# Kernel tuning notes

Hardware: AMD Instinct MI355X
Metric: run time of the kernel (lower is better)

Reference implementation:

```python
import jax, jax.numpy as jnp
import numpy as np

N_NODES = 50000


def _gcn_norm(edge_index, num_nodes):
    # PyG GCNConv default: add self-loops, symmetric normalization D^-1/2 A D^-1/2
    src, dst = edge_index[0], edge_index[1]
    loops = jnp.arange(num_nodes, dtype=src.dtype)
    src = jnp.concatenate([src, loops])
    dst = jnp.concatenate([dst, loops])
    deg = jax.ops.segment_sum(jnp.ones_like(src, dtype=jnp.float32), dst,
                              num_segments=num_nodes)
    dis = jnp.where(deg > 0, jax.lax.rsqrt(jnp.maximum(deg, 1.0)), 0.0)
    norm = dis[src] * dis[dst]  # [E']
    return src, dst, norm


def _gcn_conv(x, W, b, src, dst, norm, num_nodes):
    h = x @ W                                   # [N, out] transform first
    msg = h[src] * norm[:, None]                # [E', out] gather + scale
    agg = jax.ops.segment_sum(msg, dst, num_segments=num_nodes)  # scatter-add
    return agg + b


def setup_inputs() -> dict:
    key = jax.random.key(0)
    k1, k2, k3, k4 = jax.random.split(key, 4)
    n, e, d_in, d_h = N_NODES, 800000, 256, 128
    basic_block = jax.random.normal(k1, (n, d_in), dtype=jnp.float32)
    edge_index = jax.random.randint(k2, (2, e), 0, n, dtype=jnp.int64)
    W1 = jax.random.normal(k3, (d_in, d_h), dtype=jnp.float32) * (1.0 / np.sqrt(d_in))
    b1 = jnp.zeros((d_h,), dtype=jnp.float32)
    W2 = jax.random.normal(k4, (d_h, d_h), dtype=jnp.float32) * (1.0 / np.sqrt(d_h))
    b2 = jnp.zeros((d_h,), dtype=jnp.float32)
    return {"basic_block": basic_block, "edge_index": edge_index,
            "W1": W1, "b1": b1, "W2": W2, "b2": b2}


def reference(basic_block, edge_index, W1, b1, W2, b2):
    n = basic_block.shape[0]
    src, dst, norm = _gcn_norm(edge_index, n)
    x = jax.nn.relu(_gcn_conv(basic_block, W1, b1, src, dst, norm, n))
    x = _gcn_conv(x, W2, b2, src, dst, norm, n)
    return x
```

## Files before the change

### kernel.cpp

```cpp
#include <hip/hip_runtime.h>
#include <hip/hip_bf16.h>
#include <stdint.h>

#define D_H 128
#define CAP 64

typedef __bf16 bf16_t;
typedef unsigned short u16;
typedef bf16_t bf16x8 __attribute__((ext_vector_type(8)));
typedef bf16_t bf16x4 __attribute__((ext_vector_type(4)));
typedef float  f32x4  __attribute__((ext_vector_type(4)));

__global__ void k_pref(const int* __restrict__ src, const int* __restrict__ dst,
                       int* __restrict__ cnt, u16* __restrict__ csr,
                       int E, int gcr,
                       const float* __restrict__ W1, bf16_t* __restrict__ W1h,
                       bf16_t* __restrict__ W1l, int K1,
                       const float* __restrict__ W2, bf16_t* __restrict__ W2h,
                       bf16_t* __restrict__ W2l, int K2) {
    int bx = (int)blockIdx.x;
    if (bx < gcr) {
        int e = bx * 256 + threadIdx.x;
        if (e < E) {
            int d   = dst[e];
            int pos = atomicAdd(&cnt[d], 1);
            if (pos < CAP) csr[(size_t)d * CAP + pos] = (u16)src[e];
        }
        return;
    }
    int id = (bx - gcr) * 256 + threadIdx.x;
    int n1 = K1 * 128;
    if (id < n1) {
        int k = id >> 7, n = id & 127;
        float w = W1[id];
        bf16_t h = (bf16_t)w;
        W1h[(size_t)n * K1 + k] = h;
        W1l[(size_t)n * K1 + k] = (bf16_t)(w - (float)h);
    } else if (id < n1 + K2 * 128) {
        int id2 = id - n1;
        int k = id2 >> 7, n = id2 & 127;
        float w = W2[id2];
        bf16_t h = (bf16_t)w;
        W2h[(size_t)n * K2 + k] = h;
        W2l[(size_t)n * K2 + k] = (bf16_t)(w - (float)h);
    }
}

#define LDK 40

__global__ __launch_bounds__(256) void k_mm1(
        const float* __restrict__ Af,
        const bf16_t* __restrict__ Wh, const bf16_t* __restrict__ Wl,
        const int* __restrict__ cnt, bf16_t* __restrict__ Cb,
        int N, int K) {
    __shared__ bf16_t AsH[64][LDK];
    __shared__ bf16_t AsL[64][LDK];
    __shared__ bf16_t BsH[64][LDK];
    __shared__ bf16_t BsL[64][LDK];

    const int t    = threadIdx.x;
    const int lane = t & 63;
    const int wave = t >> 6;
    const int row0 = ((int)blockIdx.x >> 1) * 64;
    const int col0 = ((int)blockIdx.x & 1) * 64;
    const int wm   = (wave & 1) * 32;
    const int wn   = (wave >> 1) * 32;
    const int fm   = lane & 15;
    const int fq   = lane >> 4;

    f32x4 acc[2][2] = {};

    for (int k0 = 0; k0 < K; k0 += 32) {
        __syncthreads();
#pragma unroll
        for (int i = 0; i < 2; i++) {
            int idx = t + i * 256;
            int r   = idx >> 3;
            int c4  = idx & 7;
            int gr  = row0 + r;
            float4 v = make_float4(0.f, 0.f, 0.f, 0.f);
            if (gr < N) v = *(const float4*)(Af + (size_t)gr * K + k0 + c4 * 4);
            bf16_t h0 = (bf16_t)v.x, h1 = (bf16_t)v.y, h2 = (bf16_t)v.z, h3 = (bf16_t)v.w;
            bf16_t l0 = (bf16_t)(v.x - (float)h0);
            bf16_t l1 = (bf16_t)(v.y - (float)h1);
            bf16_t l2 = (bf16_t)(v.z - (float)h2);
            bf16_t l3 = (bf16_t)(v.w - (float)h3);
            *(bf16x4*)&AsH[r][c4 * 4] = (bf16x4){h0, h1, h2, h3};
            *(bf16x4*)&AsL[r][c4 * 4] = (bf16x4){l0, l1, l2, l3};
        }
        {
            int r  = t >> 2;
            int c8 = t & 3;
            *(bf16x8*)&BsH[r][c8 * 8] = *(const bf16x8*)(Wh + (size_t)(col0 + r) * K + k0 + c8 * 8);
            *(bf16x8*)&BsL[r][c8 * 8] = *(const bf16x8*)(Wl + (size_t)(col0 + r) * K + k0 + c8 * 8);
        }
        __syncthreads();

        bf16x8 ah[2], al[2], bh[2], bl[2];
#pragma unroll
        for (int i = 0; i < 2; i++) {
            ah[i] = *(const bf16x8*)&AsH[wm + i * 16 + fm][fq * 8];
            al[i] = *(const bf16x8*)&AsL[wm + i * 16 + fm][fq * 8];
            bh[i] = *(const bf16x8*)&BsH[wn + i * 16 + fm][fq * 8];
            bl[i] = *(const bf16x8*)&BsL[wn + i * 16 + fm][fq * 8];
        }
#pragma unroll
        for (int mi = 0; mi < 2; mi++)
#pragma unroll
            for (int ni = 0; ni < 2; ni++) {
                acc[mi][ni] = __builtin_amdgcn_mfma_f32_16x16x32_bf16(ah[mi], bh[ni], acc[mi][ni], 0, 0, 0);
                acc[mi][ni] = __builtin_amdgcn_mfma_f32_16x16x32_bf16(ah[mi], bl[ni], acc[mi][ni], 0, 0, 0);
                acc[mi][ni] = __builtin_amdgcn_mfma_f32_16x16x32_bf16(al[mi], bh[ni], acc[mi][ni], 0, 0, 0);
            }
    }

#pragma unroll
    for (int mi = 0; mi < 2; mi++)
#pragma unroll
        for (int r = 0; r < 4; r++) {
            int grow = row0 + wm + mi * 16 + fq * 4 + r;
            if (grow < N) {
                float dr = 1.0f / sqrtf((float)(cnt[grow] + 1));
#pragma unroll
                for (int ni = 0; ni < 2; ni++)
                    Cb[(size_t)grow * D_H + col0 + wn + ni * 16 + fm] = (bf16_t)(dr * acc[mi][ni][r]);
            }
        }
}

__global__ __launch_bounds__(256) void k_mm2(const bf16_t* __restrict__ Ah,
                                             const bf16_t* __restrict__ Al,
                                             const bf16_t* __restrict__ Wh,
                                             const bf16_t* __restrict__ Wl,
                                             const int* __restrict__ cnt,
                                             bf16_t* __restrict__ Cb,
                                             int N, int K) {
    __shared__ bf16_t AsH[64][LDK];
    __shared__ bf16_t AsL[64][LDK];
    __shared__ bf16_t BsH[64][LDK];
    __shared__ bf16_t BsL[64][LDK];

    const int t    = threadIdx.x;
    const int lane = t & 63;
    const int wave = t >> 6;
    const int row0 = ((int)blockIdx.x >> 1) * 64;
    const int col0 = ((int)blockIdx.x & 1) * 64;
    const int wm   = (wave & 1) * 32;
    const int wn   = (wave >> 1) * 32;
    const int fm   = lane & 15;
    const int fq   = lane >> 4;

    f32x4 acc[2][2] = {};

    for (int k0 = 0; k0 < K; k0 += 32) {
        __syncthreads();
        {
            int r  = t >> 2;
            int c8 = t & 3;
            int gr = row0 + r;
            bf16x8 vh = {}, vl = {};
            if (gr < N) {
                vh = *(const bf16x8*)(Ah + (size_t)gr * K + k0 + c8 * 8);
                vl = *(const bf16x8*)(Al + (size_t)gr * K + k0 + c8 * 8);
            }
            *(bf16x8*)&AsH[r][c8 * 8] = vh;
            *(bf16x8*)&AsL[r][c8 * 8] = vl;
            *(bf16x8*)&BsH[r][c8 * 8] = *(const bf16x8*)(Wh + (size_t)(col0 + r) * K + k0 + c8 * 8);
            *(bf16x8*)&BsL[r][c8 * 8] = *(const bf16x8*)(Wl + (size_t)(col0 + r) * K + k0 + c8 * 8);
        }
        __syncthreads();

        bf16x8 ah[2], al[2], bh[2], bl[2];
#pragma unroll
        for (int i = 0; i < 2; i++) {
            ah[i] = *(const bf16x8*)&AsH[wm + i * 16 + fm][fq * 8];
            al[i] = *(const bf16x8*)&AsL[wm + i * 16 + fm][fq * 8];
            bh[i] = *(const bf16x8*)&BsH[wn + i * 16 + fm][fq * 8];
            bl[i] = *(const bf16x8*)&BsL[wn + i * 16 + fm][fq * 8];
        }
#pragma unroll
        for (int mi = 0; mi < 2; mi++)
#pragma unroll
            for (int ni = 0; ni < 2; ni++) {
                acc[mi][ni] = __builtin_amdgcn_mfma_f32_16x16x32_bf16(ah[mi], bh[ni], acc[mi][ni], 0, 0, 0);
                acc[mi][ni] = __builtin_amdgcn_mfma_f32_16x16x32_bf16(ah[mi], bl[ni], acc[mi][ni], 0, 0, 0);
                acc[mi][ni] = __builtin_amdgcn_mfma_f32_16x16x32_bf16(al[mi], bh[ni], acc[mi][ni], 0, 0, 0);
            }
    }

#pragma unroll
    for (int mi = 0; mi < 2; mi++)
#pragma unroll
        for (int r = 0; r < 4; r++) {
            int grow = row0 + wm + mi * 16 + fq * 4 + r;
            if (grow < N) {
                float dr = 1.0f / sqrtf((float)(cnt[grow] + 1));
#pragma unroll
                for (int ni = 0; ni < 2; ni++)
                    Cb[(size_t)grow * D_H + col0 + wn + ni * 16 + fm] = (bf16_t)(dr * acc[mi][ni][r]);
            }
        }
}

__global__ __launch_bounds__(256) void k_agg(const bf16_t* __restrict__ Hb,
                                             const int* __restrict__ cnt,
                                             const u16* __restrict__ csr,
                                             const float4* __restrict__ bias4,
                                             float4* __restrict__ outF,
                                             bf16_t* __restrict__ outH,
                                             bf16_t* __restrict__ outL,
                                             int N, int mode) {
    const int slot = threadIdx.x >> 4;
    const int lane = threadIdx.x & 15;
    const int node = blockIdx.x * 16 + slot;
    if (node >= N) return;

    const bf16_t* Hrow = Hb + (size_t)lane * 8;
    const int  deg = min(cnt[node], CAP);
    const u16* lst = csr + (size_t)node * CAP;

    float a0[8], a1[8], a2[8], a3[8];
    {
        bf16x8 v = *(const bf16x8*)(Hrow + (size_t)node * D_H);
#pragma unroll
        for (int j = 0; j < 8; j++) { a0[j] = (float)v[j]; a1[j] = 0.f; a2[j] = 0.f; a3[j] = 0.f; }
    }

    int k = 0;
    for (; k + 4 <= deg; k += 4) {
        ushort4 s4 = *(const ushort4*)(lst + k);
        bf16x8 h0 = *(const bf16x8*)(Hrow + (size_t)s4.x * D_H);
        bf16x8 h1 = *(const bf16x8*)(Hrow + (size_t)s4.y * D_H);
        bf16x8 h2 = *(const bf16x8*)(Hrow + (size_t)s4.z * D_H);
        bf16x8 h3 = *(const bf16x8*)(Hrow + (size_t)s4.w * D_H);
#pragma unroll
        for (int j = 0; j < 8; j++) {
            a0[j] += (float)h0[j];
            a1[j] += (float)h1[j];
            a2[j] += (float)h2[j];
            a3[j] += (float)h3[j];
        }
    }
    if (k + 2 <= deg) {
        int s0 = (int)lst[k], s1 = (int)lst[k + 1];
        bf16x8 h0 = *(const bf16x8*)(Hrow + (size_t)s0 * D_H);
        bf16x8 h1 = *(const bf16x8*)(Hrow + (size_t)s1 * D_H);
#pragma unroll
        for (int j = 0; j < 8; j++) { a0[j] += (float)h0[j]; a1[j] += (float)h1[j]; }
        k += 2;
    }
    if (k < deg) {
        int s0 = (int)lst[k];
        bf16x8 h0 = *(const bf16x8*)(Hrow + (size_t)s0 * D_H);
#pragma unroll
        for (int j = 0; j < 8; j++) a2[j] += (float)h0[j];
    }

    float sum[8];
#pragma unroll
    for (int j = 0; j < 8; j++) sum[j] = (a0[j] + a1[j]) + (a2[j] + a3[j]);

    const float  di = 1.0f / sqrtf((float)(deg + 1));
    const float4 b0 = bias4[lane * 2];
    const float4 b1 = bias4[lane * 2 + 1];
    float v0 = fmaf(di, sum[0], b0.x), v1 = fmaf(di, sum[1], b0.y);
    float v2 = fmaf(di, sum[2], b0.z), v3 = fmaf(di, sum[3], b0.w);
    float v4 = fmaf(di, sum[4], b1.x), v5 = fmaf(di, sum[5], b1.y);
    float v6 = fmaf(di, sum[6], b1.z), v7 = fmaf(di, sum[7], b1.w);

    if (mode == 1) {
        v0 = fmaxf(v0, 0.f); v1 = fmaxf(v1, 0.f); v2 = fmaxf(v2, 0.f); v3 = fmaxf(v3, 0.f);
        v4 = fmaxf(v4, 0.f); v5 = fmaxf(v5, 0.f); v6 = fmaxf(v6, 0.f); v7 = fmaxf(v7, 0.f);
        bf16_t h0 = (bf16_t)v0, h1 = (bf16_t)v1, h2 = (bf16_t)v2, h3 = (bf16_t)v3;
        bf16_t h4 = (bf16_t)v4, h5 = (bf16_t)v5, h6 = (bf16_t)v6, h7 = (bf16_t)v7;
        *(bf16x8*)(outH + (size_t)node * D_H + lane * 8) =
            (bf16x8){h0, h1, h2, h3, h4, h5, h6, h7};
        *(bf16x8*)(outL + (size_t)node * D_H + lane * 8) =
            (bf16x8){(bf16_t)(v0 - (float)h0), (bf16_t)(v1 - (float)h1),
                     (bf16_t)(v2 - (float)h2), (bf16_t)(v3 - (float)h3),
                     (bf16_t)(v4 - (float)h4), (bf16_t)(v5 - (float)h5),
                     (bf16_t)(v6 - (float)h6), (bf16_t)(v7 - (float)h7)};
    } else {
        outF[(size_t)node * 32 + lane * 2]     = make_float4(v0, v1, v2, v3);
        outF[(size_t)node * 32 + lane * 2 + 1] = make_float4(v4, v5, v6, v7);
    }
}

extern "C" void kernel_launch(void* const* d_in, const int* in_sizes, int n_in,
                              void* d_out, int out_size, void* d_ws, size_t ws_size,
                              hipStream_t stream) {
    const float* X  = (const float*)d_in[0];
    const int*   ei = (const int*)d_in[1];
    const float* W1 = (const float*)d_in[2];
    const float* b1 = (const float*)d_in[3];
    const float* W2 = (const float*)d_in[4];
    const float* b2 = (const float*)d_in[5];
    float* out = (float*)d_out;

    const int N  = in_sizes[0] / 256;
    const int E  = in_sizes[1] / 2;
    const int K1 = 256;

    const int* src = ei;
    const int* dst = ei + E;

    uintptr_t p = (uintptr_t)d_ws;
    auto carve = [&](size_t bytes) {
        uintptr_t q = p;
        p += (bytes + 255) & ~(size_t)255;
        return q;
    };
    int*    cnt   = (int*)carve((size_t)N * 4);
    u16*    csr   = (u16*)carve((size_t)N * CAP * 2);
    bf16_t* Hb    = (bf16_t*)carve((size_t)N * D_H * 2);
    bf16_t* X1h   = (bf16_t*)carve((size_t)N * D_H * 2);
    bf16_t* X1l   = (bf16_t*)carve((size_t)N * D_H * 2);
    bf16_t* W1h   = (bf16_t*)carve((size_t)K1 * D_H * 2);
    bf16_t* W1l   = (bf16_t*)carve((size_t)K1 * D_H * 2);
    bf16_t* W2h   = (bf16_t*)carve((size_t)D_H * D_H * 2);
    bf16_t* W2l   = (bf16_t*)carve((size_t)D_H * D_H * 2);

    hipMemsetAsync(cnt, 0, (size_t)N * 4, stream);

    const int gcr = (E + 255) / 256;
    const int gw  = (K1 * 128 + D_H * 128 + 255) / 256;
    k_pref<<<gcr + gw, 256, 0, stream>>>(src, dst, cnt, csr, E, gcr,
                                         W1, W1h, W1l, K1,
                                         W2, W2h, W2l, D_H);

    const int gmm = ((N + 63) / 64) * 2;
    const int gag = (N + 15) / 16;

    k_mm1<<<gmm, 256, 0, stream>>>(X, W1h, W1l, cnt, Hb, N, K1);
    k_agg<<<gag, 256, 0, stream>>>(Hb, cnt, csr,
                                   (const float4*)b1, nullptr, X1h, X1l, N, 1);
    k_mm2<<<gmm, 256, 0, stream>>>(X1h, X1l, W2h, W2l, cnt, Hb, N, D_H);
    k_agg<<<gag, 256, 0, stream>>>(Hb, cnt, csr,
                                   (const float4*)b2, (float4*)out, nullptr, nullptr, N, 0);
}
```

Measured before the change: 247.0 us.

## Fuse CSR edge bucketing into first GEMM and move source normalization into aggregation

Edge bucketing (atomic counting and CSR fill) moves out of the prep kernel into the tail of the first GEMM, with edge indices loaded before the GEMM loop so their latency overlaps compute. The hipMemset is replaced by zeroing inside the weight-prep kernel. Because degrees are not known during the GEMM, the source-side D^-1/2 scaling moves into the aggregation kernel, which now reads cnt[src] per neighbor. This saves a launch and the serial bucketing pass, at the cost of extra random cnt reads and rsqrt work per edge in both aggregation passes.

```diff
diff --git a/kernel.cpp b/kernel.cpp
--- a/kernel.cpp
+++ b/kernel.cpp
@@ -11,24 +11,18 @@
 typedef bf16_t bf16x4 __attribute__((ext_vector_type(4)));
 typedef float  f32x4  __attribute__((ext_vector_type(4)));
 
-__global__ void k_pref(const int* __restrict__ src, const int* __restrict__ dst,
-                       int* __restrict__ cnt, u16* __restrict__ csr,
-                       int E, int gcr,
+__global__ void k_prew(int* __restrict__ cnt, int N, int gz,
                        const float* __restrict__ W1, bf16_t* __restrict__ W1h,
                        bf16_t* __restrict__ W1l, int K1,
                        const float* __restrict__ W2, bf16_t* __restrict__ W2h,
                        bf16_t* __restrict__ W2l, int K2) {
     int bx = (int)blockIdx.x;
-    if (bx < gcr) {
-        int e = bx * 256 + threadIdx.x;
-        if (e < E) {
-            int d   = dst[e];
-            int pos = atomicAdd(&cnt[d], 1);
-            if (pos < CAP) csr[(size_t)d * CAP + pos] = (u16)src[e];
-        }
+    if (bx < gz) {
+        int i = bx * 256 + threadIdx.x;
+        if (i < N) cnt[i] = 0;
         return;
     }
-    int id = (bx - gcr) * 256 + threadIdx.x;
+    int id = (bx - gz) * 256 + threadIdx.x;
     int n1 = K1 * 128;
     if (id < n1) {
         int k = id >> 7, n = id & 127;
@@ -47,12 +41,15 @@
 }
 
 #define LDK 40
-
-__global__ __launch_bounds__(256) void k_mm1(
+#define FILL_PER 2
+
+__global__ __launch_bounds__(256) void k_mm1fill(
         const float* __restrict__ Af,
         const bf16_t* __restrict__ Wh, const bf16_t* __restrict__ Wl,
-        const int* __restrict__ cnt, bf16_t* __restrict__ Cb,
-        int N, int K) {
+        bf16_t* __restrict__ Cb, int N, int K,
+        const int* __restrict__ src, const int* __restrict__ dst,
+        int* __restrict__ cnt, u16* __restrict__ csr,
+        int E, int totThreads) {
     __shared__ bf16_t AsH[64][LDK];
     __shared__ bf16_t AsL[64][LDK];
     __shared__ bf16_t BsH[64][LDK];
@@ -67,6 +64,16 @@
     const int wn   = (wave >> 1) * 32;
     const int fm   = lane & 15;
     const int fq   = lane >> 4;
+
+    const int g = (int)blockIdx.x * 256 + t;
+    int ed[FILL_PER];
+    int es[FILL_PER];
+#pragma unroll
+    for (int i = 0; i < FILL_PER; i++) {
+        int e = g + i * totThreads;
+        if (e < E) { ed[i] = dst[e]; es[i] = src[e]; }
+        else       { ed[i] = -1;     es[i] = 0; }
+    }
 
     f32x4 acc[2][2] = {};
 
@@ -120,11 +127,17 @@
         for (int r = 0; r < 4; r++) {
             int grow = row0 + wm + mi * 16 + fq * 4 + r;
             if (grow < N) {
-                float dr = 1.0f / sqrtf((float)(cnt[grow] + 1));
 #pragma unroll
                 for (int ni = 0; ni < 2; ni++)
-                    Cb[(size_t)grow * D_H + col0 + wn + ni * 16 + fm] = (bf16_t)(dr * acc[mi][ni][r]);
-            }
+                    Cb[(size_t)grow * D_H + col0 + wn + ni * 16 + fm] = (bf16_t)acc[mi][ni][r];
+            }
+        }
+
+#pragma unroll
+    for (int i = 0; i < FILL_PER; i++)
+        if (ed[i] >= 0) {
+            int pos = atomicAdd(&cnt[ed[i]], 1);
+            if (pos < CAP) csr[(size_t)ed[i] * CAP + pos] = (u16)es[i];
         }
 }
 
@@ -132,7 +145,6 @@
                                              const bf16_t* __restrict__ Al,
                                              const bf16_t* __restrict__ Wh,
                                              const bf16_t* __restrict__ Wl,
-                                             const int* __restrict__ cnt,
                                              bf16_t* __restrict__ Cb,
                                              int N, int K) {
     __shared__ bf16_t AsH[64][LDK];
@@ -194,10 +206,9 @@
         for (int r = 0; r < 4; r++) {
             int grow = row0 + wm + mi * 16 + fq * 4 + r;
             if (grow < N) {
-                float dr = 1.0f / sqrtf((float)(cnt[grow] + 1));
 #pragma unroll
                 for (int ni = 0; ni < 2; ni++)
-                    Cb[(size_t)grow * D_H + col0 + wn + ni * 16 + fm] = (bf16_t)(dr * acc[mi][ni][r]);
+                    Cb[(size_t)grow * D_H + col0 + wn + ni * 16 + fm] = (bf16_t)acc[mi][ni][r];
             }
         }
 }
@@ -216,57 +227,71 @@
     if (node >= N) return;
 
     const bf16_t* Hrow = Hb + (size_t)lane * 8;
-    const int  deg = min(cnt[node], CAP);
-    const u16* lst = csr + (size_t)node * CAP;
+    const int   cself = cnt[node];
+    const float dself = 1.0f / sqrtf((float)(cself + 1));
+    const int   deg   = min(cself, CAP);
+    const u16*  lst   = csr + (size_t)node * CAP;
 
     float a0[8], a1[8], a2[8], a3[8];
     {
         bf16x8 v = *(const bf16x8*)(Hrow + (size_t)node * D_H);
 #pragma unroll
-        for (int j = 0; j < 8; j++) { a0[j] = (float)v[j]; a1[j] = 0.f; a2[j] = 0.f; a3[j] = 0.f; }
+        for (int j = 0; j < 8; j++) { a0[j] = dself * (float)v[j]; a1[j] = 0.f; a2[j] = 0.f; a3[j] = 0.f; }
     }
 
     int k = 0;
     for (; k + 4 <= deg; k += 4) {
         ushort4 s4 = *(const ushort4*)(lst + k);
+        int c0 = cnt[s4.x], c1 = cnt[s4.y], c2 = cnt[s4.z], c3 = cnt[s4.w];
         bf16x8 h0 = *(const bf16x8*)(Hrow + (size_t)s4.x * D_H);
         bf16x8 h1 = *(const bf16x8*)(Hrow + (size_t)s4.y * D_H);
         bf16x8 h2 = *(const bf16x8*)(Hrow + (size_t)s4.z * D_H);
         bf16x8 h3 = *(const bf16x8*)(Hrow + (size_t)s4.w * D_H);
+        float d0 = 1.0f / sqrtf((float)(c0 + 1));
+        float d1 = 1.0f / sqrtf((float)(c1 + 1));
+        float d2 = 1.0f / sqrtf((float)(c2 + 1));
+        float d3 = 1.0f / sqrtf((float)(c3 + 1));
 #pragma unroll
         for (int j = 0; j < 8; j++) {
-            a0[j] += (float)h0[j];
-            a1[j] += (float)h1[j];
-            a2[j] += (float)h2[j];
-            a3[j] += (float)h3[j];
+            a0[j] = fmaf(d0, (float)h0[j], a0[j]);
+            a1[j] = fmaf(d1, (float)h1[j], a1[j]);
+            a2[j] = fmaf(d2, (float)h2[j], a2[j]);
+            a3[j] = fmaf(d3, (float)h3[j], a3[j]);
         }
     }
     if (k + 2 <= deg) {
         int s0 = (int)lst[k], s1 = (int)lst[k + 1];
+        int c0 = cnt[s0], c1 = cnt[s1];
         bf16x8 h0 = *(const bf16x8*)(Hrow + (size_t)s0 * D_H);
         bf16x8 h1 = *(const bf16x8*)(Hrow + (size_t)s1 * D_H);
-#pragma unroll
-        for (int j = 0; j < 8; j++) { a0[j] += (float)h0[j]; a1[j] += (float)h1[j]; }
+        float d0 = 1.0f / sqrtf((float)(c0 + 1));
+        float d1 = 1.0f / sqrtf((float)(c1 + 1));
+#pragma unroll
+        for (int j = 0; j < 8; j++) {
+            a0[j] = fmaf(d0, (float)h0[j], a0[j]);
+            a1[j] = fmaf(d1, (float)h1[j], a1[j]);
+        }
         k += 2;
     }
     if (k < deg) {
         int s0 = (int)lst[k];
+        int c0 = cnt[s0];
         bf16x8 h0 = *(const bf16x8*)(Hrow + (size_t)s0 * D_H);
-#pragma unroll
-        for (int j = 0; j < 8; j++) a2[j] += (float)h0[j];
+        float d0 = 1.0f / sqrtf((float)(c0 + 1));
+#pragma unroll
+        for (int j = 0; j < 8; j++) a2[j] = fmaf(d0, (float)h0[j], a2[j]);
     }
 
     float sum[8];
 #pragma unroll
     for (int j = 0; j < 8; j++) sum[j] = (a0[j] + a1[j]) + (a2[j] + a3[j]);
 
-    const float  di = 1.0f / sqrtf((float)(deg + 1));
     const float4 b0 = bias4[lane * 2];
     const float4 b1 = bias4[lane * 2 + 1];
-    float v0 = fmaf(di, sum[0], b0.x), v1 = fmaf(di, sum[1], b0.y);
-    float v2 = fmaf(di, sum[2], b0.z), v3 = fmaf(di, sum[3], b0.w);
-    float v4 = fmaf(di, sum[4], b1.x), v5 = fmaf(di, sum[5], b1.y);
-    float v6 = fmaf(di, sum[6], b1.z), v7 = fmaf(di, sum[7], b1.w);
+    float v0 = fmaf(dself, sum[0], b0.x), v1 = fmaf(dself, sum[1], b0.y);
+    float v2 = fmaf(dself, sum[2], b0.z), v3 = fmaf(dself, sum[3], b0.w);
+    float v4 = fmaf(dself, sum[4], b1.x), v5 = fmaf(dself, sum[5], b1.y);
+    float v6 = fmaf(dself, sum[6], b1.z), v7 = fmaf(dself, sum[7], b1.w);
 
     if (mode == 1) {
         v0 = fmaxf(v0, 0.f); v1 = fmaxf(v1, 0.f); v2 = fmaxf(v2, 0.f); v3 = fmaxf(v3, 0.f);
@@ -320,21 +345,20 @@
     bf16_t* W2h   = (bf16_t*)carve((size_t)D_H * D_H * 2);
     bf16_t* W2l   = (bf16_t*)carve((size_t)D_H * D_H * 2);
 
-    hipMemsetAsync(cnt, 0, (size_t)N * 4, stream);
-
-    const int gcr = (E + 255) / 256;
-    const int gw  = (K1 * 128 + D_H * 128 + 255) / 256;
-    k_pref<<<gcr + gw, 256, 0, stream>>>(src, dst, cnt, csr, E, gcr,
-                                         W1, W1h, W1l, K1,
-                                         W2, W2h, W2l, D_H);
+    const int gz = (N + 255) / 256;
+    const int gw = (K1 * 128 + D_H * 128 + 255) / 256;
+    k_prew<<<gz + gw, 256, 0, stream>>>(cnt, N, gz,
+                                        W1, W1h, W1l, K1,
+                                        W2, W2h, W2l, D_H);
 
     const int gmm = ((N + 63) / 64) * 2;
     const int gag = (N + 15) / 16;
 
-    k_mm1<<<gmm, 256, 0, stream>>>(X, W1h, W1l, cnt, Hb, N, K1);
+    k_mm1fill<<<gmm, 256, 0, stream>>>(X, W1h, W1l, Hb, N, K1,
+                                       src, dst, cnt, csr, E, gmm * 256);
     k_agg<<<gag, 256, 0, stream>>>(Hb, cnt, csr,
                                    (const float4*)b1, nullptr, X1h, X1l, N, 1);
-    k_mm2<<<gmm, 256, 0, stream>>>(X1h, X1l, W2h, W2l, cnt, Hb, N, D_H);
+    k_mm2<<<gmm, 256, 0, stream>>>(X1h, X1l, W2h, W2l, Hb, N, D_H);
     k_agg<<<gag, 256, 0, stream>>>(Hb, cnt, csr,
                                    (const float4*)b2, (float4*)out, nullptr, nullptr, N, 0);
 }
```

Result: slower. 260.0 us (+5.3%).
